# Kernel tuning notes

Measured on AMD Instinct MI355X. Metric: run time of the kernel, lower is better.

## Reference

```python
import jax, jax.numpy as jnp
import numpy as np

N_NODES = 100000
N_EDGES = 3200000
DIM = 16


def setup_inputs() -> dict:
    key = jax.random.key(0)
    k1, k2, k3, k4 = jax.random.split(key, 4)
    state_input = jax.random.normal(k1, (N_NODES, DIM), dtype=jnp.float32)
    row = jax.random.randint(k2, (N_EDGES,), 0, N_NODES, dtype=jnp.int32)
    col = jax.random.randint(k3, (N_EDGES,), 0, N_NODES, dtype=jnp.int32)
    edge_weights = jax.random.uniform(k4, (N_EDGES,), dtype=jnp.float32)
    return {"state_input": state_input, "row": row, "col": col,
            "edge_weights": edge_weights}


def reference(state_input, row, col, edge_weights):
    # f_eq: per-dim self dynamics, f(x) = -x  -> [N, dim]
    self_diff = -state_input

    # gather pair endpoints: x_1 = state[col], x_2 = state[row]
    # g_eq: sin(x_2 - x_1) per dim (Kuramoto-style coupling) -> [E, dim]
    neighbor_processed = jnp.sin(state_input[row] - state_input[col])

    # weight by edge weight and scatter-sum into destination nodes (col)
    aggregated_sum = jax.ops.segment_sum(
        neighbor_processed * edge_weights[:, None], col,
        num_segments=state_input.shape[0])  # [N, dim]

    # s_eq: elementwise tanh on aggregated sum
    interact_diff = jnp.tanh(aggregated_sum)

    return (self_diff + interact_diff,
            (state_input, self_diff),
            (aggregated_sum, interact_diff))
```

## Files before the change

kernel.cpp:

```cpp
#include <hip/hip_runtime.h>
#include <hip/hip_fp16.h>
#include <math.h>

#define N_NODES 100000
#define N_EDGES 3200000
#define DIM 16
#define NSZ (N_NODES * DIM)

#define NPB 128
#define NBUCK 782
#define NBLK 512
#define EPB 6256
#define MAXCAP 5120
#define CAP 4864
#define PRK 5

typedef float nvec4 __attribute__((ext_vector_type(4)));

__global__ __launch_bounds__(512)
void prep(const float* __restrict__ state, __half* __restrict__ hs,
          float* __restrict__ out) {
    int i = blockIdx.x * 512 + threadIdx.x;
    if (i >= NSZ / 4) return;
    nvec4 v = __builtin_nontemporal_load(&((const nvec4*)state)[i]);
    union { __half2 h[2]; float2 f; } u;
    u.h[0] = __floats2half2_rn(v.x, v.y);
    u.h[1] = __floats2half2_rn(v.z, v.w);
    ((float2*)hs)[i] = u.f;
    __builtin_nontemporal_store(v, &((nvec4*)(out + 1 * (size_t)NSZ))[i]);
    nvec4 nv = {-v.x, -v.y, -v.z, -v.w};
    __builtin_nontemporal_store(nv, &((nvec4*)(out + 2 * (size_t)NSZ))[i]);
}

__global__ __launch_bounds__(512)
void sort_write(const int* __restrict__ row, const int* __restrict__ col,
                const float* __restrict__ w, int* __restrict__ cnt,
                unsigned long long* __restrict__ packed) {
    __shared__ unsigned long long sbuf[EPB];
    __shared__ int cur[NBUCK];
    __shared__ int diff[NBUCK];
    __shared__ int wsum[8];
    int t = threadIdx.x, blk = blockIdx.x;
    int e0 = blk * EPB;
    int eN = e0 + EPB; if (eN > N_EDGES) eN = N_EDGES;
    int ecnt = eN - e0;
    int nch = ecnt >> 2;
    const int4*   c4p = (const int4*)(col + e0);
    const int4*   r4p = (const int4*)(row + e0);
    const float4* w4p = (const float4*)(w + e0);

    for (int j = t; j < NBUCK; j += 512) cur[j] = 0;
    __syncthreads();
    for (int i = t; i < nch; i += 512) {
        int4 c = c4p[i];
        atomicAdd(&cur[c.x >> 7], 1);
        atomicAdd(&cur[c.y >> 7], 1);
        atomicAdd(&cur[c.z >> 7], 1);
        atomicAdd(&cur[c.w >> 7], 1);
    }
    __syncthreads();
    {
        int i0 = 2 * t, i1 = 2 * t + 1;
        int v0 = (i0 < NBUCK) ? cur[i0] : 0;
        int v1 = (i1 < NBUCK) ? cur[i1] : 0;
        int p = v0 + v1, ps = p;
        #pragma unroll
        for (int d = 1; d < 64; d <<= 1) {
            int u = __shfl_up(ps, d, 64);
            if ((t & 63) >= d) ps += u;
        }
        if ((t & 63) == 63) wsum[t >> 6] = ps;
        __syncthreads();
        int wid = t >> 6, wbase = 0;
        #pragma unroll
        for (int k = 0; k < 8; ++k) wbase += (k < wid) ? wsum[k] : 0;
        int ex = wbase + ps - p;
        if (i0 < NBUCK) {
            if (v0) {
                int base = atomicAdd(&cnt[i0], v0);
                diff[i0] = i0 * MAXCAP + base - ex;
            }
            cur[i0] = ex;
        }
        if (i1 < NBUCK) {
            if (v1) {
                int base = atomicAdd(&cnt[i1], v1);
                diff[i1] = i1 * MAXCAP + base - (ex + v0);
            }
            cur[i1] = ex + v0;
        }
    }
    __syncthreads();
    for (int i = t; i < nch; i += 512) {
        int4 c = c4p[i]; int4 r = r4p[i]; float4 ww = w4p[i];
        int pos;
        pos = atomicAdd(&cur[c.x >> 7], 1);
        sbuf[pos] = ((unsigned long long)(unsigned)c.x << 47)
                  | ((unsigned long long)(unsigned)r.x << 30)
                  | (unsigned long long)(__float_as_uint(ww.x) >> 2);
        pos = atomicAdd(&cur[c.y >> 7], 1);
        sbuf[pos] = ((unsigned long long)(unsigned)c.y << 47)
                  | ((unsigned long long)(unsigned)r.y << 30)
                  | (unsigned long long)(__float_as_uint(ww.y) >> 2);
        pos = atomicAdd(&cur[c.z >> 7], 1);
        sbuf[pos] = ((unsigned long long)(unsigned)c.z << 47)
                  | ((unsigned long long)(unsigned)r.z << 30)
                  | (unsigned long long)(__float_as_uint(ww.z) >> 2);
        pos = atomicAdd(&cur[c.w >> 7], 1);
        sbuf[pos] = ((unsigned long long)(unsigned)c.w << 47)
                  | ((unsigned long long)(unsigned)r.w << 30)
                  | (unsigned long long)(__float_as_uint(ww.w) >> 2);
    }
    __syncthreads();
    for (int i = t; i < ecnt; i += 512) {
        unsigned long long pv = sbuf[i];
        int b = (int)(pv >> 54);
        __builtin_nontemporal_store(pv, &packed[diff[b] + i]);
    }
}

__global__ __launch_bounds__(1024, 8)
void aggregate(const float* __restrict__ state, const __half2* __restrict__ hs2,
               const int* __restrict__ cnt,
               const unsigned long long* __restrict__ packed,
               float* __restrict__ out) {
    __shared__ unsigned long long sbuf[CAP];
    __shared__ int s_cnt[NPB], s_start[NPB], s_cur[NPB];
    __shared__ int s_wsum;
    int nb = blockIdx.x, t = threadIdx.x;
    int q = t & 3, sub = (t >> 2) & 1, g = t >> 3;
    int beg = nb * MAXCAP;
    int end = beg + cnt[nb];
    int n = nb * NPB + g;
    bool valid = (n < N_NODES);
    float4 xx = valid ? ((const float4*)state)[n * 4 + q]
                      : make_float4(0.f, 0.f, 0.f, 0.f);
    float4 acc = {0.f, 0.f, 0.f, 0.f};
    const uint2* hsu = (const uint2*)hs2;

    for (int tbeg = beg; tbeg < end; tbeg += CAP) {
        int tend = tbeg + CAP; if (tend > end) tend = end;
        if (t < NPB) s_cnt[t] = 0;
        __syncthreads();

        unsigned long long pr[PRK];
        #pragma unroll
        for (int k = 0; k < PRK; ++k) {
            int e = tbeg + t + k * 1024;
            if (e < tend) {
                pr[k] = __builtin_nontemporal_load(&packed[e]);
                atomicAdd(&s_cnt[(unsigned)(pr[k] >> 47) & 127u], 1);
            }
        }
        __syncthreads();

        {
            int v = 0, ps = 0;
            if (t < NPB) {
                v = s_cnt[t]; ps = v;
                #pragma unroll
                for (int d = 1; d < 64; d <<= 1) {
                    int u = __shfl_up(ps, d, 64);
                    if ((t & 63) >= d) ps += u;
                }
            }
            if (t == 63) s_wsum = ps;
            __syncthreads();
            if (t < NPB) {
                int ex = ps - v + ((t >= 64) ? s_wsum : 0);
                s_start[t] = ex;
                s_cur[t] = ex;
            }
        }
        __syncthreads();

        #pragma unroll
        for (int k = 0; k < PRK; ++k) {
            int e = tbeg + t + k * 1024;
            if (e < tend) {
                int cl = (int)((pr[k] >> 47) & 127u);
                int pos = atomicAdd(&s_cur[cl], 1);
                sbuf[pos] = pr[k];
            }
        }
        __syncthreads();

        {
            int es = s_start[g], ee = s_cur[g];
            int e = es + sub;
            for (; e + 6 < ee; e += 8) {
                unsigned long long p0 = sbuf[e];
                unsigned long long p1 = sbuf[e + 2];
                unsigned long long p2 = sbuf[e + 4];
                unsigned long long p3 = sbuf[e + 6];
                uint2 h0 = hsu[(unsigned)((p0 >> 30) & 0x1FFFFu) * 4u + q];
                uint2 h1 = hsu[(unsigned)((p1 >> 30) & 0x1FFFFu) * 4u + q];
                uint2 h2 = hsu[(unsigned)((p2 >> 30) & 0x1FFFFu) * 4u + q];
                uint2 h3 = hsu[(unsigned)((p3 >> 30) & 0x1FFFFu) * 4u + q];
                #pragma unroll
                for (int j = 0; j < 4; ++j) {
                    unsigned long long p = (j == 0) ? p0 : (j == 1) ? p1
                                         : (j == 2) ? p2 : p3;
                    uint2 hb = (j == 0) ? h0 : (j == 1) ? h1
                             : (j == 2) ? h2 : h3;
                    float we = __uint_as_float(((unsigned)p & 0x3FFFFFFFu) << 2);
                    float2 lo = __half22float2(*(const __half2*)&hb.x);
                    float2 hi = __half22float2(*(const __half2*)&hb.y);
                    acc.x += __sinf(lo.x - xx.x) * we;
                    acc.y += __sinf(lo.y - xx.y) * we;
                    acc.z += __sinf(hi.x - xx.z) * we;
                    acc.w += __sinf(hi.y - xx.w) * we;
                }
            }
            for (; e < ee; e += 2) {
                unsigned long long p = sbuf[e];
                uint2 hb = hsu[(unsigned)((p >> 30) & 0x1FFFFu) * 4u + q];
                float we = __uint_as_float(((unsigned)p & 0x3FFFFFFFu) << 2);
                float2 lo = __half22float2(*(const __half2*)&hb.x);
                float2 hi = __half22float2(*(const __half2*)&hb.y);
                acc.x += __sinf(lo.x - xx.x) * we;
                acc.y += __sinf(lo.y - xx.y) * we;
                acc.z += __sinf(hi.x - xx.z) * we;
                acc.w += __sinf(hi.y - xx.w) * we;
            }
        }
        __syncthreads();
    }

    acc.x += __shfl_xor(acc.x, 4, 64); acc.y += __shfl_xor(acc.y, 4, 64);
    acc.z += __shfl_xor(acc.z, 4, 64); acc.w += __shfl_xor(acc.w, 4, 64);

    if (valid && sub == 0) {
        float4 th = make_float4(tanhf(acc.x), tanhf(acc.y),
                                tanhf(acc.z), tanhf(acc.w));
        int gdx = n * 4 + q;
        nvec4 v0 = {th.x - xx.x, th.y - xx.y, th.z - xx.z, th.w - xx.w};
        nvec4 v3 = {acc.x, acc.y, acc.z, acc.w};
        nvec4 v4 = {th.x, th.y, th.z, th.w};
        __builtin_nontemporal_store(v0, &((nvec4*)(out + 0 * (size_t)NSZ))[gdx]);
        __builtin_nontemporal_store(v3, &((nvec4*)(out + 3 * (size_t)NSZ))[gdx]);
        __builtin_nontemporal_store(v4, &((nvec4*)(out + 4 * (size_t)NSZ))[gdx]);
    }
}

__global__ __launch_bounds__(256)
void edge_kernel(const float* __restrict__ state, const int* __restrict__ row,
                 const int* __restrict__ col, const float* __restrict__ w,
                 float* __restrict__ agg) {
    int idx = blockIdx.x * blockDim.x + threadIdx.x;
    if (idx >= N_EDGES * 4) return;
    int e = idx >> 2, qq = idx & 3;
    int r = row[e], c = col[e];
    float we = w[e];
    const float4 xr = ((const float4*)state)[r * 4 + qq];
    const float4 xcv = ((const float4*)state)[c * 4 + qq];
    float* dst = agg + c * DIM + qq * 4;
    atomicAdd(dst + 0, sinf(xr.x - xcv.x) * we);
    atomicAdd(dst + 1, sinf(xr.y - xcv.y) * we);
    atomicAdd(dst + 2, sinf(xr.z - xcv.z) * we);
    atomicAdd(dst + 3, sinf(xr.w - xcv.w) * we);
}

__global__ __launch_bounds__(256)
void node_kernel(const float* __restrict__ state, const float* __restrict__ agg,
                 float* __restrict__ out) {
    int idx = blockIdx.x * blockDim.x + threadIdx.x;
    if (idx >= N_NODES * 4) return;
    float4 x = ((const float4*)state)[idx];
    float4 a = ((const float4*)agg)[idx];
    float4 tv = make_float4(tanhf(a.x), tanhf(a.y), tanhf(a.z), tanhf(a.w));
    ((float4*)(out + 0 * NSZ))[idx] = make_float4(tv.x - x.x, tv.y - x.y,
                                                  tv.z - x.z, tv.w - x.w);
    ((float4*)(out + 1 * NSZ))[idx] = x;
    ((float4*)(out + 2 * NSZ))[idx] = make_float4(-x.x, -x.y, -x.z, -x.w);
    ((float4*)(out + 4 * NSZ))[idx] = tv;
}

extern "C" void kernel_launch(void* const* d_in, const int* in_sizes, int n_in,
                              void* d_out, int out_size, void* d_ws, size_t ws_size,
                              hipStream_t stream) {
    const float* state = (const float*)d_in[0];
    const int*   row   = (const int*)d_in[1];
    const int*   col   = (const int*)d_in[2];
    const float* w     = (const float*)d_in[3];
    float* out = (float*)d_out;

    size_t packed_off = 0;
    size_t hs_off     = packed_off + (size_t)NBUCK * MAXCAP * 8;
    size_t cnt_off    = hs_off + (size_t)NSZ * 2;
    size_t needed     = cnt_off + (size_t)NBUCK * 4;

    if (ws_size >= needed) {
        unsigned long long* packed =
            (unsigned long long*)((char*)d_ws + packed_off);
        __half* hs = (__half*)((char*)d_ws + hs_off);
        int* cnt   = (int*)((char*)d_ws + cnt_off);

        (void)hipMemsetAsync(cnt, 0, (size_t)NBUCK * sizeof(int), stream);
        prep<<<(NSZ / 4 + 511) / 512, 512, 0, stream>>>(state, hs, out);
        sort_write<<<NBLK, 512, 0, stream>>>(row, col, w, cnt, packed);
        aggregate<<<NBUCK, 1024, 0, stream>>>(
            state, (const __half2*)hs, cnt, packed, out);
    } else {
        float* agg = out + 3 * NSZ;
        (void)hipMemsetAsync(agg, 0, NSZ * sizeof(float), stream);
        edge_kernel<<<(N_EDGES * 4 + 255) / 256, 256, 0, stream>>>(
            state, row, col, w, agg);
        node_kernel<<<(N_NODES * 4 + 255) / 256, 256, 0, stream>>>(
            state, agg, out);
    }
}
```

Measured before the change: 173.3 us.

## Hold packed edges in registers and scatter directly to global buckets

The bucketing kernel now loads edges once, packs them into registers, and counts buckets in that same pass. It then reserves global slots per bucket and writes each edge straight to its global position using shared-memory atomic cursors. This removes the second global read, the shared-memory staging buffer and the block-wide prefix scan. In exchange, global stores are scattered rather than grouped contiguously per bucket, which may hurt write coalescing, and each thread needs more registers.

```diff
diff --git a/kernel.cpp b/kernel.cpp
--- a/kernel.cpp
+++ b/kernel.cpp
@@ -32,90 +32,62 @@
     __builtin_nontemporal_store(nv, &((nvec4*)(out + 2 * (size_t)NSZ))[i]);
 }
 
+#define PACK(c, r, ww) (((unsigned long long)(unsigned)(c) << 47)             \
+                      | ((unsigned long long)(unsigned)(r) << 30)             \
+                      | (unsigned long long)(__float_as_uint(ww) >> 2))
+
 __global__ __launch_bounds__(512)
 void sort_write(const int* __restrict__ row, const int* __restrict__ col,
                 const float* __restrict__ w, int* __restrict__ cnt,
                 unsigned long long* __restrict__ packed) {
-    __shared__ unsigned long long sbuf[EPB];
     __shared__ int cur[NBUCK];
-    __shared__ int diff[NBUCK];
-    __shared__ int wsum[8];
     int t = threadIdx.x, blk = blockIdx.x;
     int e0 = blk * EPB;
     int eN = e0 + EPB; if (eN > N_EDGES) eN = N_EDGES;
-    int ecnt = eN - e0;
-    int nch = ecnt >> 2;
+    int nch = (eN - e0) >> 2;
     const int4*   c4p = (const int4*)(col + e0);
     const int4*   r4p = (const int4*)(row + e0);
     const float4* w4p = (const float4*)(w + e0);
 
     for (int j = t; j < NBUCK; j += 512) cur[j] = 0;
     __syncthreads();
-    for (int i = t; i < nch; i += 512) {
-        int4 c = c4p[i];
-        atomicAdd(&cur[c.x >> 7], 1);
-        atomicAdd(&cur[c.y >> 7], 1);
-        atomicAdd(&cur[c.z >> 7], 1);
-        atomicAdd(&cur[c.w >> 7], 1);
+
+    unsigned long long pr[16];
+    #pragma unroll
+    for (int k = 0; k < 4; ++k) {
+        int i = t + k * 512;
+        if (i < nch) {
+            int4 c = c4p[i]; int4 r = r4p[i]; float4 ww = w4p[i];
+            pr[4 * k + 0] = PACK(c.x, r.x, ww.x);
+            pr[4 * k + 1] = PACK(c.y, r.y, ww.y);
+            pr[4 * k + 2] = PACK(c.z, r.z, ww.z);
+            pr[4 * k + 3] = PACK(c.w, r.w, ww.w);
+            atomicAdd(&cur[c.x >> 7], 1);
+            atomicAdd(&cur[c.y >> 7], 1);
+            atomicAdd(&cur[c.z >> 7], 1);
+            atomicAdd(&cur[c.w >> 7], 1);
+        }
     }
     __syncthreads();
-    {
-        int i0 = 2 * t, i1 = 2 * t + 1;
-        int v0 = (i0 < NBUCK) ? cur[i0] : 0;
-        int v1 = (i1 < NBUCK) ? cur[i1] : 0;
-        int p = v0 + v1, ps = p;
-        #pragma unroll
-        for (int d = 1; d < 64; d <<= 1) {
-            int u = __shfl_up(ps, d, 64);
-            if ((t & 63) >= d) ps += u;
-        }
-        if ((t & 63) == 63) wsum[t >> 6] = ps;
-        __syncthreads();
-        int wid = t >> 6, wbase = 0;
-        #pragma unroll
-        for (int k = 0; k < 8; ++k) wbase += (k < wid) ? wsum[k] : 0;
-        int ex = wbase + ps - p;
-        if (i0 < NBUCK) {
-            if (v0) {
-                int base = atomicAdd(&cnt[i0], v0);
-                diff[i0] = i0 * MAXCAP + base - ex;
-            }
-            cur[i0] = ex;
-        }
-        if (i1 < NBUCK) {
-            if (v1) {
-                int base = atomicAdd(&cnt[i1], v1);
-                diff[i1] = i1 * MAXCAP + base - (ex + v0);
-            }
-            cur[i1] = ex + v0;
-        }
+
+    for (int j = t; j < NBUCK; j += 512) {
+        int v = cur[j];
+        if (v) cur[j] = j * MAXCAP + atomicAdd(&cnt[j], v);
     }
     __syncthreads();
-    for (int i = t; i < nch; i += 512) {
-        int4 c = c4p[i]; int4 r = r4p[i]; float4 ww = w4p[i];
-        int pos;
-        pos = atomicAdd(&cur[c.x >> 7], 1);
-        sbuf[pos] = ((unsigned long long)(unsigned)c.x << 47)
-                  | ((unsigned long long)(unsigned)r.x << 30)
-                  | (unsigned long long)(__float_as_uint(ww.x) >> 2);
-        pos = atomicAdd(&cur[c.y >> 7], 1);
-        sbuf[pos] = ((unsigned long long)(unsigned)c.y << 47)
-                  | ((unsigned long long)(unsigned)r.y << 30)
-                  | (unsigned long long)(__float_as_uint(ww.y) >> 2);
-        pos = atomicAdd(&cur[c.z >> 7], 1);
-        sbuf[pos] = ((unsigned long long)(unsigned)c.z << 47)
-                  | ((unsigned long long)(unsigned)r.z << 30)
-                  | (unsigned long long)(__float_as_uint(ww.z) >> 2);
-        pos = atomicAdd(&cur[c.w >> 7], 1);
-        sbuf[pos] = ((unsigned long long)(unsigned)c.w << 47)
-                  | ((unsigned long long)(unsigned)r.w << 30)
-                  | (unsigned long long)(__float_as_uint(ww.w) >> 2);
-    }
-    __syncthreads();
-    for (int i = t; i < ecnt; i += 512) {
-        unsigned long long pv = sbuf[i];
-        int b = (int)(pv >> 54);
-        __builtin_nontemporal_store(pv, &packed[diff[b] + i]);
+
+    #pragma unroll
+    for (int k = 0; k < 4; ++k) {
+        int i = t + k * 512;
+        if (i < nch) {
+            #pragma unroll
+            for (int j = 0; j < 4; ++j) {
+                unsigned long long pv = pr[4 * k + j];
+                int b = (int)(pv >> 54);
+                int pos = atomicAdd(&cur[b], 1);
+                packed[pos] = pv;
+            }
+        }
     }
 }
 
```

Measured after the change: 162.0 us. -6.5%, faster.
